# Kernel optimization log

Hardware: AMD Instinct MI355X
Metric: run time of the kernel (lower is better)

Reference implementation:

```python
import jax, jax.numpy as jnp
import numpy as np

N = 50000
DEG = 16
E = N * DEG
IN_F, HID, OUT_F = 512, 128, 64
SLOPE = 0.2


def setup_inputs() -> dict:
    key = jax.random.key(0)
    ks = jax.random.split(key, 10)
    row_ptr = jnp.arange(N + 1, dtype=jnp.int64) * DEG          # uniform-degree CSR
    col_idx = jax.random.randint(ks[0], (E,), 0, N, dtype=jnp.int64)
    x = jax.random.normal(ks[1], (N, IN_F), dtype=jnp.float32)
    s1 = 1.0 / np.sqrt(IN_F)
    s2 = 1.0 / np.sqrt(HID)
    return {
        "row_ptr": row_ptr,
        "col_idx": col_idx,
        "input_feature": x,
        "W1": jax.random.normal(ks[2], (IN_F, HID), dtype=jnp.float32) * s1,
        "attn_l1": jax.random.normal(ks[3], (HID,), dtype=jnp.float32) * s2,
        "attn_r1": jax.random.normal(ks[4], (HID,), dtype=jnp.float32) * s2,
        "bias1": jnp.zeros((HID,), dtype=jnp.float32),
        "W2": jax.random.normal(ks[5], (HID, OUT_F), dtype=jnp.float32) * s2,
        "attn_l2": jax.random.normal(ks[6], (OUT_F,), dtype=jnp.float32) * 0.125,
        "attn_r2": jax.random.normal(ks[7], (OUT_F,), dtype=jnp.float32) * 0.125,
        "bias2": jnp.zeros((OUT_F,), dtype=jnp.float32),
    }


def gat_layer(row_ptr, col_idx, x, W, attn_l, attn_r, bias):
    n = row_ptr.shape[0] - 1
    e = col_idx.shape[0]
    h = x @ W                                   # [N, F] dense GEMM
    el = h @ attn_l                             # [N] dst attention term
    er = h @ attn_r                             # [N] src attention term
    # edge -> destination row via CSR row_ptr
    dst = jnp.searchsorted(row_ptr, jnp.arange(e, dtype=row_ptr.dtype), side="right") - 1
    src = col_idx
    score = jax.nn.leaky_relu(el[dst] + er[src], negative_slope=SLOPE)  # [E]
    # neighborhood softmax over edges sharing a destination
    smax = jax.ops.segment_max(score, dst, num_segments=n)
    ex = jnp.exp(score - smax[dst])
    ssum = jax.ops.segment_sum(ex, dst, num_segments=n)
    alpha = ex / ssum[dst]                      # [E]
    # weighted gather-scatter aggregation
    out = jax.ops.segment_sum(alpha[:, None] * h[src], dst, num_segments=n)
    return out + bias


def reference(row_ptr, col_idx, input_feature, W1, attn_l1, attn_r1, bias1,
              W2, attn_l2, attn_r2, bias2):
    x = gat_layer(row_ptr, col_idx, input_feature, W1, attn_l1, attn_r1, bias1)
    x = gat_layer(row_ptr, col_idx, x, W2, attn_l2, attn_r2, bias2)
    return x
```

## Files before the change

### kernel.cpp

```cpp
#include <hip/hip_runtime.h>
#include <hip/hip_bf16.h>

#define Nn 50000
#define DEG 16
#define IN_F 512
#define HID 128
#define OUT_F 64
#define SLOPE 0.2f

typedef __attribute__((ext_vector_type(8))) short bf16x8;
typedef __attribute__((ext_vector_type(4))) float f32x4;
typedef __attribute__((ext_vector_type(2))) float f32x2;
typedef __attribute__((ext_vector_type(4))) unsigned int u32x4;

__device__ __forceinline__ unsigned short f2bf(float f) {
    return __builtin_bit_cast(unsigned short, __float2bfloat16(f));
}
__device__ __forceinline__ float bf2f(unsigned short u) {
    return __bfloat162float(__builtin_bit_cast(__hip_bfloat16, u));
}

__global__ void __launch_bounds__(256) prep_kernel(
        const float* __restrict__ W1, const float* __restrict__ W2,
        const int* __restrict__ row_ptr,
        unsigned short* __restrict__ w1t, unsigned short* __restrict__ w2t,
        int* __restrict__ flag64) {
    int g = blockIdx.x * 256 + threadIdx.x;
    if (g == 0) {
        *flag64 = (row_ptr[1] == DEG) ? 0 : 1;
    }
    if (g < IN_F * HID) {
        int k = g >> 7, c = g & 127;
        w1t[c * IN_F + k] = f2bf(W1[g]);
    } else {
        int g2 = g - IN_F * HID;
        if (g2 < HID * OUT_F) {
            int k = g2 >> 6, c = g2 & 63;
            w2t[c * HID + k] = f2bf(W2[g2]);
        }
    }
}

template<int K, int F>
__global__ void __launch_bounds__(256, 3) gemm1_reg(
        const float* __restrict__ Af, const unsigned short* __restrict__ WT,
        const float* __restrict__ alv, const float* __restrict__ arv,
        unsigned short* __restrict__ Hb, float* __restrict__ el,
        float* __restrict__ er, int M) {
    constexpr int NT  = F / 16;
    constexpr int NKS = K / 32;
    const int tid  = threadIdx.x;
    const int lane = tid & 63;
    const int w    = tid >> 6;
    const int ln   = lane & 15, q = lane >> 4;
    const int mb   = blockIdx.x * 64 + w * 16;

    int m0 = mb + ln; if (m0 > M - 1) m0 = M - 1;
    const float* a0p = Af + (size_t)m0 * K;
    const unsigned short* bp = WT + (size_t)ln * K + q * 8;

    f32x4 acc[NT] = {};

    f32x4  va0 = *(const f32x4*)(a0p + q * 8);
    f32x4  va1 = *(const f32x4*)(a0p + q * 8 + 4);
    bf16x8 bn[NT];
    #pragma unroll
    for (int nt = 0; nt < NT; ++nt)
        bn[nt] = *(const bf16x8*)(bp + (size_t)nt * 16 * K);

    #pragma unroll
    for (int ks = 0; ks < NKS; ++ks) {
        f32x4  ca0 = va0, ca1 = va1;
        bf16x8 bc[NT];
        #pragma unroll
        for (int nt = 0; nt < NT; ++nt) bc[nt] = bn[nt];
        const int kn  = (ks + 1 < NKS) ? ks + 1 : ks;
        const int kkn = kn * 32;
        va0 = *(const f32x4*)(a0p + kkn + q * 8);
        va1 = *(const f32x4*)(a0p + kkn + q * 8 + 4);
        #pragma unroll
        for (int nt = 0; nt < NT; ++nt)
            bn[nt] = *(const bf16x8*)(bp + (size_t)nt * 16 * K + kkn);
        bf16x8 af;
        #pragma unroll
        for (int jj = 0; jj < 4; ++jj) {
            af[jj]     = (short)f2bf(ca0[jj]);
            af[jj + 4] = (short)f2bf(ca1[jj]);
        }
        #pragma unroll
        for (int nt = 0; nt < NT; ++nt)
            acc[nt] = __builtin_amdgcn_mfma_f32_16x16x32_bf16(af, bc[nt], acc[nt], 0, 0, 0);
    }

    float av[NT], bv[NT];
    #pragma unroll
    for (int nt = 0; nt < NT; ++nt) {
        av[nt] = alv[nt * 16 + ln];
        bv[nt] = arv[nt * 16 + ln];
    }
    #pragma unroll
    for (int r = 0; r < 4; ++r) {
        float sl = 0.f, sr = 0.f;
        #pragma unroll
        for (int nt = 0; nt < NT; ++nt) {
            float v = acc[nt][r];
            sl += v * av[nt];
            sr += v * bv[nt];
        }
        #pragma unroll
        for (int m = 1; m < 16; m <<= 1) {
            sl += __shfl_xor(sl, m);
            sr += __shfl_xor(sr, m);
        }
        int grow = mb + q * 4 + r;
        if (grow < M) {
            #pragma unroll
            for (int nt = 0; nt < NT; ++nt)
                Hb[(size_t)grow * F + nt * 16 + ln] = f2bf(acc[nt][r]);
            if (ln == 0) { el[grow] = sl; er[grow] = sr; }
        }
    }
}

__global__ void __launch_bounds__(256) fused_agg_gemm2(
        const int* __restrict__ col, const int* __restrict__ flag64,
        const float* __restrict__ el1, const float* __restrict__ er1,
        const unsigned short* __restrict__ Hb, const float* __restrict__ b1,
        const unsigned short* __restrict__ w2t,
        const float* __restrict__ al2, const float* __restrict__ ar2,
        unsigned short* __restrict__ H2, float* __restrict__ el2,
        float* __restrict__ er2) {
    constexpr int STR = 136;
    __shared__ unsigned short at[16 * STR];
    __shared__ float redl[16][4];
    __shared__ float redr[16][4];

    const int tid  = threadIdx.x;
    const int lane = tid & 63;
    const int w    = tid >> 6;
    const int ln   = lane & 15, q = lane >> 4;
    const int nb   = blockIdx.x * 16;
    const int use64 = *flag64;

    {
        int node = nb + w * 4 + q;
        int e    = node * DEG + ln;
        int src  = use64 ? (int)((const long long*)col)[e] : col[e];
        float sc = el1[node] + er1[src];
        sc = sc >= 0.f ? sc : SLOPE * sc;
        float mx = sc;
        #pragma unroll
        for (int m = 1; m < 16; m <<= 1) mx = fmaxf(mx, __shfl_xor(mx, m, 16));
        float ex = __expf(sc - mx);
        float sm = ex;
        #pragma unroll
        for (int m = 1; m < 16; m <<= 1) sm += __shfl_xor(sm, m, 16);
        float alpha = ex / sm;

        float a[8] = {};
        #pragma unroll
        for (int jj = 0; jj < DEG; ++jj) {
            int   sl_ = q * 16 + jj;
            int   sj = __shfl(src, sl_);
            float aj = __shfl(alpha, sl_);
            bf16x8 hv = *(const bf16x8*)&Hb[(size_t)sj * HID + ln * 8];
            #pragma unroll
            for (int c = 0; c < 8; ++c)
                a[c] += aj * bf2f((unsigned short)hv[c]);
        }
        unsigned int pk[4];
        #pragma unroll
        for (int c = 0; c < 4; ++c) {
            float lo = a[2 * c]     + b1[ln * 8 + 2 * c];
            float hi = a[2 * c + 1] + b1[ln * 8 + 2 * c + 1];
            pk[c] = (unsigned int)f2bf(lo) | ((unsigned int)f2bf(hi) << 16);
        }
        *(u32x4*)&at[(w * 4 + q) * STR + ln * 8] = *(u32x4*)pk;
    }
    __syncthreads();

    f32x4 acc = {};
    const unsigned short* bb = w2t + (size_t)(w * 16 + ln) * HID;
    #pragma unroll
    for (int ks = 0; ks < HID / 32; ++ks) {
        bf16x8 af  = *(const bf16x8*)&at[ln * STR + ks * 32 + q * 8];
        bf16x8 bfr = *(const bf16x8*)&bb[ks * 32 + q * 8];
        acc = __builtin_amdgcn_mfma_f32_16x16x32_bf16(af, bfr, acc, 0, 0, 0);
    }

    float av = al2[w * 16 + ln], bv = ar2[w * 16 + ln];
    #pragma unroll
    for (int r = 0; r < 4; ++r) {
        float v  = acc[r];
        float sl = v * av, sr = v * bv;
        #pragma unroll
        for (int m = 1; m < 16; m <<= 1) {
            sl += __shfl_xor(sl, m, 16);
            sr += __shfl_xor(sr, m, 16);
        }
        int rowl = q * 4 + r;
        H2[(size_t)(nb + rowl) * OUT_F + w * 16 + ln] = f2bf(v);
        if (ln == 0) { redl[rowl][w] = sl; redr[rowl][w] = sr; }
    }
    __syncthreads();
    if (tid < 16) {
        el2[nb + tid] = redl[tid][0] + redl[tid][1] + redl[tid][2] + redl[tid][3];
        er2[nb + tid] = redr[tid][0] + redr[tid][1] + redr[tid][2] + redr[tid][3];
    }
}

__global__ void __launch_bounds__(256) agg2_k(
        const int* __restrict__ col, const int* __restrict__ flag64,
        const float* __restrict__ el, const float* __restrict__ er,
        const unsigned short* __restrict__ Hb, const float* __restrict__ bias,
        float* __restrict__ out) {
    int lane = threadIdx.x & 63;
    int node = blockIdx.x * 4 + (threadIdx.x >> 6);
    int j    = lane & 15;
    int e    = node * DEG + j;
    int src  = (*flag64) ? (int)((const long long*)col)[e] : col[e];
    float sc = el[node] + er[src];
    sc = sc >= 0.f ? sc : SLOPE * sc;
    float mx = sc;
    #pragma unroll
    for (int m = 1; m < 16; m <<= 1) mx = fmaxf(mx, __shfl_xor(mx, m, 16));
    float ex = __expf(sc - mx);
    float sm = ex;
    #pragma unroll
    for (int m = 1; m < 16; m <<= 1) sm += __shfl_xor(sm, m, 16);
    float alpha = ex / sm;

    int h = lane >> 5;
    int c = lane & 31;
    float a0 = 0.f, a1 = 0.f;
    #pragma unroll
    for (int jj = 0; jj < DEG; jj += 2) {
        int   sj = __shfl(src, jj + h, 16);
        float aj = __shfl(alpha, jj + h, 16);
        unsigned int hv = *(const unsigned int*)&Hb[(size_t)sj * OUT_F + c * 2];
        a0 += aj * bf2f((unsigned short)(hv & 0xffffu));
        a1 += aj * bf2f((unsigned short)(hv >> 16));
    }
    a0 += __shfl_xor(a0, 32);
    a1 += __shfl_xor(a1, 32);
    if (h == 0) {
        f32x2 o;
        o[0] = a0 + bias[c * 2];
        o[1] = a1 + bias[c * 2 + 1];
        *(f32x2*)&out[(size_t)node * OUT_F + c * 2] = o;
    }
}

extern "C" void kernel_launch(void* const* d_in, const int* in_sizes, int n_in,
                              void* d_out, int out_size, void* d_ws, size_t ws_size,
                              hipStream_t stream) {
    const int*   row_ptr = (const int*)d_in[0];
    const int*   col_idx = (const int*)d_in[1];
    const float* x   = (const float*)d_in[2];
    const float* W1  = (const float*)d_in[3];
    const float* al1 = (const float*)d_in[4];
    const float* ar1 = (const float*)d_in[5];
    const float* b1  = (const float*)d_in[6];
    const float* W2  = (const float*)d_in[7];
    const float* al2 = (const float*)d_in[8];
    const float* ar2 = (const float*)d_in[9];
    const float* b2  = (const float*)d_in[10];
    float* out = (float*)d_out;

    float* ws = (float*)d_ws;
    unsigned short* h1b = (unsigned short*)ws;
    unsigned short* h2b = (unsigned short*)(ws + 3200000);
    float* el1 = ws + 5000000;
    float* er1 = ws + 5050000;
    float* el2 = ws + 5100000;
    float* er2 = ws + 5150000;
    unsigned short* w1t = (unsigned short*)(ws + 5200000);
    unsigned short* w2t = (unsigned short*)(ws + 5232768);
    int* flag64 = (int*)(ws + 5236864);

    prep_kernel<<<(IN_F * HID + HID * OUT_F + 255) / 256, 256, 0, stream>>>(
        W1, W2, row_ptr, w1t, w2t, flag64);

    gemm1_reg<512, 128><<<(Nn + 63) / 64, 256, 0, stream>>>(
        x, w1t, al1, ar1, h1b, el1, er1, Nn);

    fused_agg_gemm2<<<Nn / 16, 256, 0, stream>>>(
        col_idx, flag64, el1, er1, h1b, b1, w2t, al2, ar2, h2b, el2, er2);

    agg2_k<<<Nn / 4, 256, 0, stream>>>(col_idx, flag64, el2, er2, h2b, b2, out);
}
```

Measured before the change: 265.7 us.

## Stage W1 chunks into swizzled LDS via async global-to-LDS copies in GEMM1

GEMM1 used to have every wave read W1 fragments straight from global memory into registers with software prefetch. Now the transposed W1 is pre-laid out in 128-wide K chunks with an XOR swizzle. Each block copies a 32 KB chunk into shared memory with global_load_lds and the four waves read their B fragments from LDS. This is meant to cut redundant global/L2 traffic for the weights and avoid bank conflicts, at the cost of two barriers per chunk, no overlap between the chunk load and compute, and a 32 KB LDS footprint that may lower occupancy.

```diff
diff --git a/kernel.cpp b/kernel.cpp
--- a/kernel.cpp
+++ b/kernel.cpp
@@ -19,11 +19,16 @@
 __device__ __forceinline__ float bf2f(unsigned short u) {
     return __bfloat162float(__builtin_bit_cast(__hip_bfloat16, u));
 }
+__device__ __forceinline__ void async_copy16(const void* g, void* l) {
+    __builtin_amdgcn_global_load_lds(
+        (const __attribute__((address_space(1))) unsigned int*)g,
+        (__attribute__((address_space(3))) unsigned int*)l, 16, 0, 0);
+}
 
 __global__ void __launch_bounds__(256) prep_kernel(
         const float* __restrict__ W1, const float* __restrict__ W2,
         const int* __restrict__ row_ptr,
-        unsigned short* __restrict__ w1t, unsigned short* __restrict__ w2t,
+        unsigned short* __restrict__ w1c, unsigned short* __restrict__ w2t,
         int* __restrict__ flag64) {
     int g = blockIdx.x * 256 + threadIdx.x;
     if (g == 0) {
@@ -31,7 +36,10 @@
     }
     if (g < IN_F * HID) {
         int k = g >> 7, c = g & 127;
-        w1t[c * IN_F + k] = f2bf(W1[g]);
+        int ch = k >> 7, kl = k & 127;
+        int s  = kl >> 3, j = kl & 7;
+        int sp = s ^ (c & 7);
+        w1c[ch * 16384 + c * 128 + sp * 8 + j] = f2bf(W1[g]);
     } else {
         int g2 = g - IN_F * HID;
         if (g2 < HID * OUT_F) {
@@ -41,14 +49,17 @@
     }
 }
 
-template<int K, int F>
-__global__ void __launch_bounds__(256, 3) gemm1_reg(
-        const float* __restrict__ Af, const unsigned short* __restrict__ WT,
+template<int K>
+__global__ void __launch_bounds__(256) gemm1_lds(
+        const float* __restrict__ Af, const unsigned short* __restrict__ w1c,
         const float* __restrict__ alv, const float* __restrict__ arv,
         unsigned short* __restrict__ Hb, float* __restrict__ el,
         float* __restrict__ er, int M) {
-    constexpr int NT  = F / 16;
-    constexpr int NKS = K / 32;
+    constexpr int F   = 128;
+    constexpr int NT  = 8;
+    constexpr int NCH = K / 128;
+    __shared__ unsigned short bt[128 * 128];
+
     const int tid  = threadIdx.x;
     const int lane = tid & 63;
     const int w    = tid >> 6;
@@ -57,39 +68,42 @@
 
     int m0 = mb + ln; if (m0 > M - 1) m0 = M - 1;
     const float* a0p = Af + (size_t)m0 * K;
-    const unsigned short* bp = WT + (size_t)ln * K + q * 8;
 
     f32x4 acc[NT] = {};
 
-    f32x4  va0 = *(const f32x4*)(a0p + q * 8);
-    f32x4  va1 = *(const f32x4*)(a0p + q * 8 + 4);
-    bf16x8 bn[NT];
-    #pragma unroll
-    for (int nt = 0; nt < NT; ++nt)
-        bn[nt] = *(const bf16x8*)(bp + (size_t)nt * 16 * K);
-
-    #pragma unroll
-    for (int ks = 0; ks < NKS; ++ks) {
-        f32x4  ca0 = va0, ca1 = va1;
-        bf16x8 bc[NT];
-        #pragma unroll
-        for (int nt = 0; nt < NT; ++nt) bc[nt] = bn[nt];
-        const int kn  = (ks + 1 < NKS) ? ks + 1 : ks;
-        const int kkn = kn * 32;
-        va0 = *(const f32x4*)(a0p + kkn + q * 8);
-        va1 = *(const f32x4*)(a0p + kkn + q * 8 + 4);
-        #pragma unroll
-        for (int nt = 0; nt < NT; ++nt)
-            bn[nt] = *(const bf16x8*)(bp + (size_t)nt * 16 * K + kkn);
-        bf16x8 af;
-        #pragma unroll
-        for (int jj = 0; jj < 4; ++jj) {
-            af[jj]     = (short)f2bf(ca0[jj]);
-            af[jj + 4] = (short)f2bf(ca1[jj]);
-        }
-        #pragma unroll
-        for (int nt = 0; nt < NT; ++nt)
-            acc[nt] = __builtin_amdgcn_mfma_f32_16x16x32_bf16(af, bc[nt], acc[nt], 0, 0, 0);
+    for (int ch = 0; ch < NCH; ++ch) {
+        const char* gch = (const char*)w1c + ch * 32768;
+        #pragma unroll
+        for (int i = 0; i < 8; ++i) {
+            int slot = w * 8 + i;
+            async_copy16(gch + slot * 1024 + lane * 16, (char*)bt + slot * 1024);
+        }
+        __syncthreads();
+
+        f32x4 ap[4][2];
+        #pragma unroll
+        for (int ks = 0; ks < 4; ++ks) {
+            const int kk = ch * 128 + ks * 32 + q * 8;
+            ap[ks][0] = *(const f32x4*)(a0p + kk);
+            ap[ks][1] = *(const f32x4*)(a0p + kk + 4);
+        }
+        #pragma unroll
+        for (int ks = 0; ks < 4; ++ks) {
+            bf16x8 af;
+            #pragma unroll
+            for (int jj = 0; jj < 4; ++jj) {
+                af[jj]     = (short)f2bf(ap[ks][0][jj]);
+                af[jj + 4] = (short)f2bf(ap[ks][1][jj]);
+            }
+            #pragma unroll
+            for (int nt = 0; nt < NT; ++nt) {
+                const int c  = nt * 16 + ln;
+                const int sp = (ks * 4 + q) ^ (ln & 7);
+                bf16x8 bfr = *(const bf16x8*)&bt[c * 128 + sp * 8];
+                acc[nt] = __builtin_amdgcn_mfma_f32_16x16x32_bf16(af, bfr, acc[nt], 0, 0, 0);
+            }
+        }
+        __syncthreads();
     }
 
     float av[NT], bv[NT];
@@ -274,15 +288,15 @@
     float* er1 = ws + 5050000;
     float* el2 = ws + 5100000;
     float* er2 = ws + 5150000;
-    unsigned short* w1t = (unsigned short*)(ws + 5200000);
+    unsigned short* w1c = (unsigned short*)(ws + 5200000);
     unsigned short* w2t = (unsigned short*)(ws + 5232768);
     int* flag64 = (int*)(ws + 5236864);
 
     prep_kernel<<<(IN_F * HID + HID * OUT_F + 255) / 256, 256, 0, stream>>>(
-        W1, W2, row_ptr, w1t, w2t, flag64);
-
-    gemm1_reg<512, 128><<<(Nn + 63) / 64, 256, 0, stream>>>(
-        x, w1t, al1, ar1, h1b, el1, er1, Nn);
+        W1, W2, row_ptr, w1c, w2t, flag64);
+
+    gemm1_lds<512><<<(Nn + 63) / 64, 256, 0, stream>>>(
+        x, w1c, al1, ar1, h1b, el1, er1, Nn);
 
     fused_agg_gemm2<<<Nn / 16, 256, 0, stream>>>(
         col_idx, flag64, el1, er1, h1b, b1, w2t, al2, ar2, h2b, el2, er2);
```

New measurement: 235.2 us. 11.5% less time.
